# Kernel optimization log

Hardware: AMD Instinct MI355X
Metric: run time of the kernel (lower is better)

Reference implementation:

```python
import jax, jax.numpy as jnp
import numpy as np

V, E, D_ENC, H, A, NF, K = 96, 64, 256, 256, 128, 10, 5
B, T_ENC, T_TGT = 64, 1024, 256


def setup_inputs() -> dict:
    key = jax.random.key(0)
    ks = jax.random.split(key, 16)
    s = 0.05
    emb = jax.random.normal(ks[0], (V, E), jnp.float32) * s
    emb = emb.at[0].set(0.0)  # padding_idx=0
    inp = {
        "encoder_outputs": jax.random.normal(ks[1], (B, T_ENC, D_ENC), jnp.float32),
        "encoder_lengths": jax.random.randint(ks[2], (B,), 1, T_ENC + 1),
        "targets": jax.random.randint(ks[3], (B, T_TGT), 0, V),
        "emb": emb,
        "W_ih": jax.random.normal(ks[4], (4 * H, E + D_ENC), jnp.float32) * s,
        "W_hh": jax.random.normal(ks[5], (4 * H, H), jnp.float32) * s,
        "b_ih": jax.random.normal(ks[6], (4 * H,), jnp.float32) * s,
        "b_hh": jax.random.normal(ks[7], (4 * H,), jnp.float32) * s,
        "conv_w": jax.random.normal(ks[8], (NF, 1, K), jnp.float32) * s,
        "W_enc": jax.random.normal(ks[9], (A, D_ENC), jnp.float32) * s,
        "W_dec": jax.random.normal(ks[10], (A, H), jnp.float32) * s,
        "W_loc": jax.random.normal(ks[11], (A, NF), jnp.float32) * s,
        "v_w": jax.random.normal(ks[12], (1, A), jnp.float32) * s,
        "out_w1": jax.random.normal(ks[13], (H, H + D_ENC), jnp.float32) * s,
        "out_b1": jax.random.normal(ks[14], (H,), jnp.float32) * s,
        "out_w2": jax.random.normal(ks[15], (V, H), jnp.float32) * s,
        "out_b2": jnp.zeros((V,), jnp.float32),
    }
    return inp


def _forward(encoder_outputs, encoder_lengths, targets, emb, W_ih, W_hh, b_ih,
             b_hh, conv_w, W_enc, W_dec, W_loc, v_w, out_w1, out_b1, out_w2, out_b2):
    dtype = encoder_outputs.dtype
    b, t_enc, d_enc = encoder_outputs.shape
    mask = jnp.arange(t_enc)[None, :] < encoder_lengths[:, None]  # [B, T_enc]
    enc_proj = encoder_outputs @ W_enc.T  # [B, T_enc, A] (weights fixed -> hoisted)
    bias = b_ih + b_hh
    pad = (K - 1) // 2

    tok_emb = emb[targets[:, :-1]]          # [B, T_dec, E]
    tok_emb = jnp.swapaxes(tok_emb, 0, 1)   # [T_dec, B, E] for scan

    h0 = jnp.zeros((b, H), dtype)
    c0 = jnp.zeros((b, H), dtype)
    ctx0 = jnp.zeros((b, d_enc), dtype)
    aw0 = jnp.full((b, t_enc), 1.0 / t_enc, dtype)

    def step(carry, e_t):
        h, c, ctx, aw = carry
        # LSTM cell (PyTorch gate order i, f, g, o)
        x = jnp.concatenate([e_t, ctx], axis=-1)            # [B, E+D_enc]
        gates = x @ W_ih.T + h @ W_hh.T + bias              # [B, 4H]
        i, f, g, o = jnp.split(gates, 4, axis=-1)
        c = jax.nn.sigmoid(f) * c + jax.nn.sigmoid(i) * jnp.tanh(g)
        h = jax.nn.sigmoid(o) * jnp.tanh(c)
        # location-sensitive attention
        loc = jax.lax.conv_general_dilated(aw[:, None, :], conv_w, (1,),
                                           [(pad, pad)],
                                           dimension_numbers=("NCH", "OIH", "NCH"))
        loc = jnp.swapaxes(loc, 1, 2)                       # [B, T_enc, NF]
        energy_in = enc_proj + (h @ W_dec.T)[:, None, :] + loc @ W_loc.T
        energy = jnp.tanh(energy_in) @ v_w[0]               # [B, T_enc]
        energy = jnp.where(mask, energy, -1e9)
        aw = jax.nn.softmax(energy, axis=1)
        ctx = jnp.einsum("bt,btd->bd", aw, encoder_outputs)
        # output MLP (dropout = identity at eval)
        hid = jnp.tanh(jnp.concatenate([h, ctx], axis=-1) @ out_w1.T + out_b1)
        logits = hid @ out_w2.T + out_b2                    # [B, V]
        return (h, c, ctx, aw), logits

    _, logits = jax.lax.scan(step, (h0, c0, ctx0, aw0), tok_emb)
    return jnp.swapaxes(logits, 0, 1)  # [B, T_dec, V]


def reference(encoder_outputs, encoder_lengths, targets, emb, W_ih, W_hh, b_ih,
              b_hh, conv_w, W_enc, W_dec, W_loc, v_w, out_w1, out_b1, out_w2, out_b2):
    return _forward(encoder_outputs, encoder_lengths, targets, emb, W_ih, W_hh,
                    b_ih, b_hh, conv_w, W_enc, W_dec, W_loc, v_w, out_w1,
                    out_b1, out_w2, out_b2)
```

## Files before the change

### kernel.cpp

```cpp
#include <hip/hip_runtime.h>
#include <hip/hip_bf16.h>

#define BB   64
#define TENC 1024
#define DENC 256
#define HN   256
#define AN   128
#define NFC  10
#define EMBD 64
#define VN   96
#define TT   255
#define KX   576

__device__ __forceinline__ float fsig(float x){ return 1.0f/(1.0f+__expf(-x)); }
__device__ __forceinline__ float ftanh(float x){ return 1.0f - 2.0f/(1.0f+__expf(2.0f*x)); }

__global__ void k_prep(const float* __restrict__ W_ih, const float* __restrict__ W_hh,
                       const float* __restrict__ b_ih, const float* __restrict__ b_hh,
                       const float* __restrict__ W_dec,
                       float* __restrict__ Wcomb, float* __restrict__ bias,
                       float* __restrict__ WdecT, float* __restrict__ e_init,
                       float* __restrict__ S_init)
{
    int tid = blockIdx.x*blockDim.x + threadIdx.x;
    int total = blockDim.x*gridDim.x;
    for (int i = tid; i < 1024*KX; i += total){
        int g = i / KX, k = i - g*KX;
        Wcomb[i] = (k < 320) ? W_ih[g*320 + k] : W_hh[g*256 + (k-320)];
    }
    for (int i = tid; i < 1024; i += total) bias[i] = b_ih[i] + b_hh[i];
    for (int i = tid; i < 256*128; i += total){ int u = i>>7, a = i&127; WdecT[i] = W_dec[a*256 + u]; }
    for (int i = tid; i < BB*TENC; i += total) e_init[i] = 1.0f;
    for (int i = tid; i < BB; i += total) S_init[i] = (float)TENC;
}

__global__ __launch_bounds__(128) void k_encproj(const float* __restrict__ enc,
                                                 const float* __restrict__ W_enc,
                                                 float* __restrict__ enc_proj)
{
    __shared__ float rows[32][256];
    int r0 = blockIdx.x * 32;
    for (int i = threadIdx.x; i < 32*256; i += 128)
        rows[i>>8][i&255] = enc[(size_t)r0*256 + i];
    __syncthreads();
    int a = threadIdx.x;
    float acc[32];
    #pragma unroll
    for (int r=0;r<32;r++) acc[r]=0.f;
    const float* w = W_enc + a*256;
    for (int d=0; d<256; d+=4){
        float4 wv = *(const float4*)(w + d);
        #pragma unroll
        for (int r=0;r<32;r++){
            float4 rv = *(const float4*)(&rows[r][d]);
            acc[r] += wv.x*rv.x + wv.y*rv.y + wv.z*rv.z + wv.w*rv.w;
        }
    }
    for (int r=0;r<32;r++) enc_proj[(size_t)(r0+r)*AN + a] = acc[r];
}

__global__ __launch_bounds__(256) void k_att(
    const float* __restrict__ enc, const float* __restrict__ enc_proj,
    const float* __restrict__ conv_w, const float* __restrict__ W_loc,
    const float* __restrict__ v_w, const int* __restrict__ lengths,
    const float* __restrict__ WdecT, const float* __restrict__ h_cur,
    const float* __restrict__ e_prev, float* __restrict__ e_new,
    const float* __restrict__ SU_r, float* __restrict__ ctxU_w, float* __restrict__ SU_w)
{
    int b  = blockIdx.y;
    int ch = blockIdx.x;
    int t0 = ch*64;
    int tid = threadIdx.x;

    int len = lengths[b];
    int nv = len - t0; nv = nv < 0 ? 0 : (nv > 64 ? 64 : nv);
    if (nv == 0){
        if (tid < 64) e_new[b*TENC + t0 + tid] = 0.f;
        return;
    }

    __shared__ float hdec_s[128];
    __shared__ float part_s[256];
    __shared__ float ehalo[68];
    __shared__ float loc_s[64][11];
    __shared__ float cw_s[52];
    __shared__ float evals[64];
    __shared__ float ep[64][33];
    __shared__ float wacc[4][256];

    if (tid < 50) cw_s[tid] = conv_w[tid];
    for (int i = tid; i < 68; i += 256){
        int g = t0 - 2 + i;
        ehalo[i] = (g >= 0 && g < TENC) ? e_prev[b*TENC + g] : 0.f;
    }
    {
        int a = tid & 127, half = tid >> 7;
        const float* wd = WdecT + (size_t)(half*128)*AN + a;
        const float* hb = h_cur + b*HN + half*128;
        float s0 = 0.f, s1 = 0.f;
        for (int u = 0; u < 128; u += 2){
            s0 += hb[u]   * wd[(size_t)u*AN];
            s1 += hb[u+1] * wd[(size_t)(u+1)*AN];
        }
        part_s[tid] = s0 + s1;
    }
    __syncthreads();
    if (tid < 128) hdec_s[tid] = part_s[tid] + part_s[tid+128];
    float invS = 1.0f / SU_r[b];
    if (tid < 64){
        int p = tid;
        #pragma unroll
        for (int f = 0; f < NFC; f++){
            float s = 0.f;
            #pragma unroll
            for (int k = 0; k < 5; k++) s += ehalo[p+k] * cw_s[f*5+k];
            loc_s[p][f] = s * invS;
        }
    }
    __syncthreads();

    {
        int ag = tid & 31, pg = tid >> 5;
        int a0 = ag*4;
        float4 hd = *(const float4*)&hdec_s[a0];
        float4 vv = *(const float4*)(v_w + a0);
        float4 wl[NFC];
        #pragma unroll
        for (int f = 0; f < NFC; f++){
            wl[f].x = W_loc[(a0+0)*NFC + f];
            wl[f].y = W_loc[(a0+1)*NFC + f];
            wl[f].z = W_loc[(a0+2)*NFC + f];
            wl[f].w = W_loc[(a0+3)*NFC + f];
        }
        for (int i = 0; i < 8; i++){
            int p = pg*8 + i;
            if (p < nv){
                float4 er = *(const float4*)(enc_proj + (size_t)(b*TENC + t0 + p)*AN + a0);
                float x0 = er.x + hd.x, x1 = er.y + hd.y, x2 = er.z + hd.z, x3 = er.w + hd.w;
                #pragma unroll
                for (int f = 0; f < NFC; f++){
                    float lf = loc_s[p][f];
                    x0 += lf * wl[f].x; x1 += lf * wl[f].y;
                    x2 += lf * wl[f].z; x3 += lf * wl[f].w;
                }
                ep[p][ag] = vv.x*ftanh(x0) + vv.y*ftanh(x1) + vv.z*ftanh(x2) + vv.w*ftanh(x3);
            }
        }
    }
    __syncthreads();

    if (tid < 64){
        int p = tid;
        float e = 0.f;
        if (p < nv){
            float s0 = 0.f, s1 = 0.f;
            #pragma unroll
            for (int j = 0; j < 32; j += 2){ s0 += ep[p][j]; s1 += ep[p][j+1]; }
            e = __expf(s0 + s1);
        }
        evals[p] = e;
        e_new[b*TENC + t0 + p] = e;
        float se = e;
        #pragma unroll
        for (int off = 32; off; off >>= 1) se += __shfl_xor(se, off);
        if (tid == 0) atomicAdd(SU_w + b, se);
    }
    __syncthreads();

    {
        int dq = tid & 63, pq = tid >> 6;
        float4 acc = {0.f,0.f,0.f,0.f};
        for (int i = 0; i < 16; i++){
            int p = pq + i*4;
            if (p < nv){
                float ev = evals[p];
                float4 ex = *(const float4*)(enc + (size_t)(b*TENC + t0 + p)*DENC + dq*4);
                acc.x += ev*ex.x; acc.y += ev*ex.y; acc.z += ev*ex.z; acc.w += ev*ex.w;
            }
        }
        *(float4*)&wacc[pq][dq*4] = acc;
    }
    __syncthreads();
    {
        int d = tid;
        float s = wacc[0][d] + wacc[1][d] + wacc[2][d] + wacc[3][d];
        atomicAdd(ctxU_w + b*DENC + d, s);
    }
}

__global__ __launch_bounds__(256) void k_cell(
    const float* __restrict__ ctxU_r, const float* __restrict__ SU_r,
    float* __restrict__ ctxU_w, float* __restrict__ SU_w,
    const int* __restrict__ targets, const float* __restrict__ emb,
    const float* __restrict__ Wcomb, const float* __restrict__ bias,
    const float* __restrict__ h_old, float* __restrict__ h_new, float* __restrict__ c_st,
    const float* __restrict__ out_w1, const float* __restrict__ out_b1,
    const float* __restrict__ hid_prev, float* __restrict__ hid_new,
    const float* __restrict__ out_w2, const float* __restrict__ out_b2,
    float* __restrict__ out, int t)
{
    int blk = blockIdx.x, tid = threadIdx.x;
    bool do_reduce = (t >= 1 && t <= 255);
    bool do_gates  = (t <= 254);
    bool do_hid    = (t >= 1 && t <= 255);
    bool do_logits = (t >= 2);

    __shared__ float smem[16*580];
    __shared__ float invS_s[32];
    __shared__ float gates_s[16][17];

    if (blk < 256){
        int bg = blk >> 6, ug = blk & 63;
        int b0 = bg*16;
        if (ug == 1 && t <= 254){
            for (int i = tid; i < 16*DENC; i += 256) ctxU_w[b0*DENC + i] = 0.f;
            if (tid < 16) SU_w[b0 + tid] = 0.f;
        }
        if (!do_gates) return;
        float (*xh)[580] = (float(*)[580])smem;
        if (tid < 16) invS_s[tid] = do_reduce ? 1.0f/SU_r[b0+tid] : 0.f;
        for (int i = tid; i < 16*EMBD; i += 256){
            int bl = i>>6, j = i&63;
            int tok = targets[(b0+bl)*256 + t];
            xh[bl][j] = emb[tok*EMBD + j];
        }
        for (int i = tid; i < 16*HN; i += 256){
            int bl = i>>8, d = i&255;
            xh[bl][320+d] = (t == 0) ? 0.f : h_old[(b0+bl)*HN + d];
        }
        __syncthreads();
        for (int i = tid; i < 16*DENC; i += 256){
            int bl = i>>8, d = i&255;
            xh[bl][64+d] = do_reduce ? ctxU_r[(b0+bl)*DENC + d] * invS_s[bl] : 0.f;
        }
        __syncthreads();
        {
            int bl = tid & 15, row = tid >> 4;
            int gidx = row >> 2, ul = row & 3;
            int g = gidx*256 + ug*4 + ul;
            const float* wr = Wcomb + (size_t)g*KX;
            float a0 = bias[g], a1 = 0.f, a2 = 0.f, a3 = 0.f;
            for (int k = 0; k < KX; k += 4){
                float4 wv = *(const float4*)(wr + k);
                float4 xv = *(const float4*)(&xh[bl][k]);
                a0 += wv.x*xv.x; a1 += wv.y*xv.y; a2 += wv.z*xv.z; a3 += wv.w*xv.w;
            }
            gates_s[bl][row] = (a0+a1)+(a2+a3);
        }
        __syncthreads();
        if (tid < 64){
            int bl = tid >> 2, ul = tid & 3;
            int bgl = b0 + bl, ugl = ug*4 + ul;
            float gi = gates_s[bl][0*4+ul], gf = gates_s[bl][1*4+ul];
            float gg = gates_s[bl][2*4+ul], go = gates_s[bl][3*4+ul];
            float cold = (t == 0) ? 0.f : c_st[bgl*HN + ugl];
            float cn = fsig(gf)*cold + fsig(gi)*ftanh(gg);
            c_st[bgl*HN + ugl] = cn;
            h_new[bgl*HN + ugl] = fsig(go)*ftanh(cn);
        }
        return;
    }

    if (blk < 320){
        if (!do_hid) return;
        int hb = blk - 256;
        int bg = hb >> 4, rg = hb & 15;
        int b0 = bg*16;
        float (*xh2)[516] = (float(*)[516])smem;
        if (tid < 16) invS_s[tid] = 1.0f/SU_r[b0+tid];
        for (int i = tid; i < 16*HN; i += 256){
            int bl = i>>8, d = i&255;
            xh2[bl][d] = h_old[(b0+bl)*HN + d];
        }
        __syncthreads();
        for (int i = tid; i < 16*DENC; i += 256){
            int bl = i>>8, d = i&255;
            xh2[bl][256+d] = ctxU_r[(b0+bl)*DENC + d] * invS_s[bl];
        }
        __syncthreads();
        {
            int bl = tid & 15, rl = tid >> 4;
            int r = rg*16 + rl;
            const float* w1 = out_w1 + (size_t)r*512;
            float a0 = 0.f, a1 = 0.f, a2 = 0.f, a3 = 0.f;
            for (int k = 0; k < 512; k += 4){
                float4 wv = *(const float4*)(w1 + k);
                float4 xv = *(const float4*)(&xh2[bl][k]);
                a0 += wv.x*xv.x; a1 += wv.y*xv.y; a2 += wv.z*xv.z; a3 += wv.w*xv.w;
            }
            hid_new[(b0+bl)*HN + r] = ftanh(((a0+a1)+(a2+a3)) + out_b1[r]);
        }
        return;
    }

    {
        if (!do_logits) return;
        int lb = blk - 320;
        int vg = lb % 12, bgr = lb / 12;
        int b0 = bgr*32;
        float (*hs)[260] = (float(*)[260])smem;
        for (int i = tid; i < 32*HN; i += 256){
            int bl = i>>8, d = i&255;
            hs[bl][d] = hid_prev[(b0+bl)*HN + d];
        }
        __syncthreads();
        {
            int bl = tid & 31, vr = tid >> 5;
            int v = vg*8 + vr;
            const float* w2 = out_w2 + (size_t)v*HN;
            float a0 = 0.f, a1 = 0.f, a2 = 0.f, a3 = 0.f;
            for (int k = 0; k < HN; k += 4){
                float4 wv = *(const float4*)(w2 + k);
                float4 xv = *(const float4*)(&hs[bl][k]);
                a0 += wv.x*xv.x; a1 += wv.y*xv.y; a2 += wv.z*xv.z; a3 += wv.w*xv.w;
            }
            out[((size_t)(b0+bl)*TT + (t-2))*VN + v] = ((a0+a1)+(a2+a3)) + out_b2[v];
        }
    }
}

extern "C" void kernel_launch(void* const* d_in, const int* in_sizes, int n_in,
                              void* d_out, int out_size, void* d_ws, size_t ws_size,
                              hipStream_t stream)
{
    const float* enc     = (const float*)d_in[0];
    const int*   lengths = (const int*)  d_in[1];
    const int*   targets = (const int*)  d_in[2];
    const float* emb     = (const float*)d_in[3];
    const float* W_ih    = (const float*)d_in[4];
    const float* W_hh    = (const float*)d_in[5];
    const float* b_ih    = (const float*)d_in[6];
    const float* b_hh    = (const float*)d_in[7];
    const float* conv_w  = (const float*)d_in[8];
    const float* W_enc   = (const float*)d_in[9];
    const float* W_dec   = (const float*)d_in[10];
    const float* W_loc   = (const float*)d_in[11];
    const float* v_w     = (const float*)d_in[12];
    const float* out_w1  = (const float*)d_in[13];
    const float* out_b1  = (const float*)d_in[14];
    const float* out_w2  = (const float*)d_in[15];
    const float* out_b2  = (const float*)d_in[16];
    float* out = (float*)d_out;

    float* ws = (float*)d_ws;
    size_t off = 0;
    auto alloc = [&](size_t n){ float* p = ws + off; off += n; return p; };
    float* enc_proj = alloc((size_t)BB*TENC*AN);
    float* Wcomb    = alloc(1024*KX);
    float* biasw    = alloc(1024);
    float* WdecT    = alloc(256*128);
    float* e0       = alloc(BB*TENC);
    float* e1       = alloc(BB*TENC);
    float* ebuf[2]  = {e0, e1};
    float* ctxU0    = alloc(BB*DENC);
    float* ctxU1    = alloc(BB*DENC);
    float* ctxU[2]  = {ctxU0, ctxU1};
    float* SU0      = alloc(BB);
    float* SU1      = alloc(BB);
    float* SU[2]    = {SU0, SU1};
    float* h0       = alloc(BB*HN);
    float* h1       = alloc(BB*HN);
    float* hbuf[2]  = {h0, h1};
    float* c_st     = alloc(BB*HN);
    float* hidA     = alloc(BB*HN);
    float* hidB     = alloc(BB*HN);
    float* hidbuf[2] = {hidA, hidB};
    if (off * sizeof(float) > ws_size) return;

    k_prep<<<dim3(512), dim3(256), 0, stream>>>(W_ih, W_hh, b_ih, b_hh, W_dec,
                                                Wcomb, biasw, WdecT, e1, SU1);
    k_encproj<<<dim3(2048), dim3(128), 0, stream>>>(enc, W_enc, enc_proj);

    for (int t = 0; t <= 256; t++){
        k_cell<<<dim3(344), dim3(256), 0, stream>>>(
            ctxU[(t+1)&1], SU[(t+1)&1], ctxU[t&1], SU[t&1],
            targets, emb, Wcomb, biasw,
            hbuf[(t+1)&1], hbuf[t&1], c_st,
            out_w1, out_b1, hidbuf[(t+1)&1], hidbuf[t&1],
            out_w2, out_b2, out, t);
        if (t <= 254){
            k_att<<<dim3(16,64), dim3(256), 0, stream>>>(
                enc, enc_proj, conv_w, W_loc, v_w, lengths, WdecT,
                hbuf[t&1], ebuf[(t+1)&1], ebuf[t&1],
                SU[(t+1)&1], ctxU[t&1], SU[t&1]);
        }
    }
}
```

Before: 11.72 ms.

## Fuse decoder time loop into one persistent cooperative kernel with grid syncs

Replaces about 512 per-step kernel launches with one persistent cooperative kernel of 256 blocks. Each step runs a cell phase and an attention phase separated by grid-wide barriers. Weights are pre-transposed so the gate, output-MLP and logits matvecs read coalesced columns and split the K dimension across warps. Each block now handles four attention chunks, which cuts parallelism to 256 blocks in exchange for removing launch overhead. If the cooperative launch fails, the code falls back to per-step launches.

```diff
diff --git a/kernel.cpp b/kernel.cpp
--- a/kernel.cpp
+++ b/kernel.cpp
@@ -1,5 +1,8 @@
 #include <hip/hip_runtime.h>
 #include <hip/hip_bf16.h>
+#include <hip/hip_cooperative_groups.h>
+
+namespace cg = cooperative_groups;
 
 #define BB   64
 #define TENC 1024
@@ -10,28 +13,44 @@
 #define EMBD 64
 #define VN   96
 #define TT   255
-#define KX   576
 
 __device__ __forceinline__ float fsig(float x){ return 1.0f/(1.0f+__expf(-x)); }
 __device__ __forceinline__ float ftanh(float x){ return 1.0f - 2.0f/(1.0f+__expf(2.0f*x)); }
 
+struct Params {
+    const float* enc; const float* enc_proj;
+    const float* conv_w; const float* W_loc; const float* v_w;
+    const int* lengths; const int* targets; const float* emb;
+    const float* WdecT; const float* WcombP; const float* biasw;
+    const float* W1T; const float* out_b1; const float* W2T; const float* out_b2;
+    float* e0; float* e1; float* ctxU0; float* ctxU1; float* SU0; float* SU1;
+    float* h0; float* h1; float* c_st; float* hidA; float* hidB;
+    float* out;
+};
+
 __global__ void k_prep(const float* __restrict__ W_ih, const float* __restrict__ W_hh,
                        const float* __restrict__ b_ih, const float* __restrict__ b_hh,
-                       const float* __restrict__ W_dec,
-                       float* __restrict__ Wcomb, float* __restrict__ bias,
-                       float* __restrict__ WdecT, float* __restrict__ e_init,
+                       const float* __restrict__ W_dec, const float* __restrict__ out_w1,
+                       const float* __restrict__ out_w2,
+                       float* __restrict__ WcombP, float* __restrict__ biasw,
+                       float* __restrict__ WdecT, float* __restrict__ W1T,
+                       float* __restrict__ W2T, float* __restrict__ e_init,
                        float* __restrict__ S_init)
 {
     int tid = blockIdx.x*blockDim.x + threadIdx.x;
-    int total = blockDim.x*gridDim.x;
-    for (int i = tid; i < 1024*KX; i += total){
-        int g = i / KX, k = i - g*KX;
-        Wcomb[i] = (k < 320) ? W_ih[g*320 + k] : W_hh[g*256 + (k-320)];
-    }
-    for (int i = tid; i < 1024; i += total) bias[i] = b_ih[i] + b_hh[i];
-    for (int i = tid; i < 256*128; i += total){ int u = i>>7, a = i&127; WdecT[i] = W_dec[a*256 + u]; }
-    for (int i = tid; i < BB*TENC; i += total) e_init[i] = 1.0f;
-    for (int i = tid; i < BB; i += total) S_init[i] = (float)TENC;
+    int tot = blockDim.x*gridDim.x;
+    for (int i = tid; i < 576*1024; i += tot){
+        int k = i >> 10, rp = i & 1023;
+        int ug = rp >> 4, q = rp & 15, gidx = q >> 2, ul = q & 3;
+        int g = gidx*256 + ug*4 + ul;
+        WcombP[i] = (k < 320) ? W_ih[(size_t)g*320 + k] : W_hh[(size_t)g*256 + (k-320)];
+    }
+    for (int i = tid; i < 1024; i += tot) biasw[i] = b_ih[i] + b_hh[i];
+    for (int i = tid; i < 256*128; i += tot){ int u = i>>7, a = i&127; WdecT[i] = W_dec[a*256 + u]; }
+    for (int i = tid; i < 512*256; i += tot){ int k = i>>8, r = i&255; W1T[i] = out_w1[(size_t)r*512 + k]; }
+    for (int i = tid; i < 256*96;  i += tot){ int k = i/96, v = i - k*96; W2T[i] = out_w2[(size_t)v*256 + k]; }
+    for (int i = tid; i < BB*TENC; i += tot) e_init[i] = 1.0f;
+    for (int i = tid; i < BB; i += tot) S_init[i] = (float)TENC;
 }
 
 __global__ __launch_bounds__(128) void k_encproj(const float* __restrict__ enc,
@@ -59,264 +78,306 @@
     for (int r=0;r<32;r++) enc_proj[(size_t)(r0+r)*AN + a] = acc[r];
 }
 
-__global__ __launch_bounds__(256) void k_att(
-    const float* __restrict__ enc, const float* __restrict__ enc_proj,
-    const float* __restrict__ conv_w, const float* __restrict__ W_loc,
-    const float* __restrict__ v_w, const int* __restrict__ lengths,
-    const float* __restrict__ WdecT, const float* __restrict__ h_cur,
-    const float* __restrict__ e_prev, float* __restrict__ e_new,
-    const float* __restrict__ SU_r, float* __restrict__ ctxU_w, float* __restrict__ SU_w)
-{
-    int b  = blockIdx.y;
-    int ch = blockIdx.x;
-    int t0 = ch*64;
-    int tid = threadIdx.x;
-
-    int len = lengths[b];
-    int nv = len - t0; nv = nv < 0 ? 0 : (nv > 64 ? 64 : nv);
-    if (nv == 0){
-        if (tid < 64) e_new[b*TENC + t0 + tid] = 0.f;
-        return;
-    }
-
-    __shared__ float hdec_s[128];
-    __shared__ float part_s[256];
-    __shared__ float ehalo[68];
-    __shared__ float loc_s[64][11];
-    __shared__ float cw_s[52];
-    __shared__ float evals[64];
-    __shared__ float ep[64][33];
-    __shared__ float wacc[4][256];
-
-    if (tid < 50) cw_s[tid] = conv_w[tid];
-    for (int i = tid; i < 68; i += 256){
-        int g = t0 - 2 + i;
-        ehalo[i] = (g >= 0 && g < TENC) ? e_prev[b*TENC + g] : 0.f;
-    }
+union alignas(16) SMem {
+    struct { float hdec[128]; float part[256]; float ehalo[68]; float loc[64][11];
+             float cw[52]; float evals[64]; float ep[64][33]; float wacc[4][256]; } att;
+    struct { float xh[8][584]; float part[4][16][9]; float gates[8][17]; } gat;
+    struct { float xh[8][520]; float part[4][16][9]; } hidm;
+    struct { float hs[8][260]; float part[4][32][9]; } lgt;
+};
+
+__device__ __forceinline__ void cell_phase(const Params& P, int t, int blk, int tid, SMem& u)
+{
+    const int wr = t & 1;
+    const float* ctxU_r = wr ? P.ctxU0 : P.ctxU1;
+    float*       ctxU_w = wr ? P.ctxU1 : P.ctxU0;
+    const float* SU_r   = wr ? P.SU0   : P.SU1;
+    float*       SU_w   = wr ? P.SU1   : P.SU0;
+    const float* h_old  = wr ? P.h0    : P.h1;
+    float*       h_new  = wr ? P.h1    : P.h0;
+    const float* hid_pv = wr ? P.hidA  : P.hidB;
+    float*       hid_nw = wr ? P.hidB  : P.hidA;
+
+    for (int half = 0; half < 2; half++){
+        if (t > 254) break;
+        const int vb = blk + (half << 8);
+        const int ug = vb & 63, bg = vb >> 6;
+        const int b0 = bg*8;
+        if (ug == 1){
+            for (int i = tid; i < 8*DENC; i += 256) ctxU_w[b0*DENC + i] = 0.f;
+            if (tid < 8) SU_w[b0 + tid] = 0.f;
+        }
+        for (int i = tid; i < 8*EMBD; i += 256){
+            int bl = i>>6, j = i&63;
+            int tok = P.targets[(b0+bl)*256 + t];
+            u.gat.xh[bl][j] = P.emb[tok*EMBD + j];
+        }
+        for (int i = tid; i < 8*HN; i += 256){
+            int bl = i>>8, d = i&255;
+            u.gat.xh[bl][320+d] = (t == 0) ? 0.f : h_old[(b0+bl)*HN + d];
+        }
+        for (int i = tid; i < 8*DENC; i += 256){
+            int bl = i>>8, d = i&255;
+            u.gat.xh[bl][64+d] = (t == 0) ? 0.f
+                : ctxU_r[(b0+bl)*DENC + d] * (1.0f/SU_r[b0+bl]);
+        }
+        __syncthreads();
+        {
+            const int kq = tid >> 6, lane = tid & 63, rl = lane & 15, blq = lane >> 4;
+            const int rowP = ug*16 + rl, bl0 = blq*2;
+            const float* wp  = P.WcombP + (size_t)(kq*144)*1024 + rowP;
+            const float* x0p = &u.gat.xh[bl0][kq*144];
+            const float* x1p = &u.gat.xh[bl0+1][kq*144];
+            float s0 = 0.f, s1 = 0.f;
+            for (int k = 0; k < 144; k += 4){
+                float w0 = wp[0], w1 = wp[1024], w2 = wp[2048], w3 = wp[3072]; wp += 4096;
+                float4 xa = *(const float4*)(x0p + k);
+                float4 xb = *(const float4*)(x1p + k);
+                s0 += w0*xa.x + w1*xa.y + w2*xa.z + w3*xa.w;
+                s1 += w0*xb.x + w1*xb.y + w2*xb.z + w3*xb.w;
+            }
+            u.gat.part[kq][rl][bl0] = s0; u.gat.part[kq][rl][bl0+1] = s1;
+        }
+        __syncthreads();
+        if (tid < 128){
+            int bl = tid >> 4, rl = tid & 15;
+            float s = u.gat.part[0][rl][bl] + u.gat.part[1][rl][bl]
+                    + u.gat.part[2][rl][bl] + u.gat.part[3][rl][bl];
+            int gidx = rl >> 2, ul = rl & 3;
+            u.gat.gates[bl][rl] = s + P.biasw[gidx*256 + ug*4 + ul];
+        }
+        __syncthreads();
+        if (tid < 32){
+            int bl = tid >> 2, ul = tid & 3;
+            int bgl = b0 + bl, unit = ug*4 + ul;
+            float gi = u.gat.gates[bl][0+ul],  gf = u.gat.gates[bl][4+ul];
+            float gg = u.gat.gates[bl][8+ul],  go = u.gat.gates[bl][12+ul];
+            float cold = (t == 0) ? 0.f : P.c_st[bgl*HN + unit];
+            float cn = fsig(gf)*cold + fsig(gi)*ftanh(gg);
+            P.c_st[bgl*HN + unit] = cn;
+            h_new[bgl*HN + unit] = fsig(go)*ftanh(cn);
+        }
+        __syncthreads();
+    }
+
+    if (blk < 128 && t >= 1 && t <= 255){
+        int bg = blk >> 4, rg = blk & 15;
+        int b0 = bg*8, r0 = rg*16;
+        for (int i = tid; i < 8*HN; i += 256){
+            int bl = i>>8, d = i&255;
+            u.hidm.xh[bl][d] = h_old[(b0+bl)*HN + d];
+        }
+        for (int i = tid; i < 8*DENC; i += 256){
+            int bl = i>>8, d = i&255;
+            u.hidm.xh[bl][256+d] = ctxU_r[(b0+bl)*DENC + d] * (1.0f/SU_r[b0+bl]);
+        }
+        __syncthreads();
+        {
+            const int kq = tid >> 6, lane = tid & 63, rl = lane & 15, blq = lane >> 4;
+            const int bl0 = blq*2;
+            const float* wp  = P.W1T + (size_t)(kq*128)*256 + (r0 + rl);
+            const float* x0p = &u.hidm.xh[bl0][kq*128];
+            const float* x1p = &u.hidm.xh[bl0+1][kq*128];
+            float s0 = 0.f, s1 = 0.f;
+            for (int k = 0; k < 128; k += 4){
+                float w0 = wp[0], w1 = wp[256], w2 = wp[512], w3 = wp[768]; wp += 1024;
+                float4 xa = *(const float4*)(x0p + k);
+                float4 xb = *(const float4*)(x1p + k);
+                s0 += w0*xa.x + w1*xa.y + w2*xa.z + w3*xa.w;
+                s1 += w0*xb.x + w1*xb.y + w2*xb.z + w3*xb.w;
+            }
+            u.hidm.part[kq][rl][bl0] = s0; u.hidm.part[kq][rl][bl0+1] = s1;
+        }
+        __syncthreads();
+        if (tid < 128){
+            int bl = tid >> 4, rl = tid & 15;
+            int r = r0 + rl;
+            float s = u.hidm.part[0][rl][bl] + u.hidm.part[1][rl][bl]
+                    + u.hidm.part[2][rl][bl] + u.hidm.part[3][rl][bl];
+            hid_nw[(b0+bl)*HN + r] = ftanh(s + P.out_b1[r]);
+        }
+        __syncthreads();
+    }
+
+    if (blk >= 128 && blk < 152 && t >= 2){
+        int lt = blk - 128;
+        int bgr = lt/3, vg = lt%3;
+        int b0 = bgr*8, v0 = vg*32;
+        for (int i = tid; i < 8*HN; i += 256){
+            int bl = i>>8, d = i&255;
+            u.lgt.hs[bl][d] = hid_pv[(b0+bl)*HN + d];
+        }
+        __syncthreads();
+        {
+            const int kq = tid >> 6, lane = tid & 63, vl = lane & 31, blq = lane >> 5;
+            const int bl0 = blq*4;
+            const float* wp = P.W2T + (size_t)(kq*64)*96 + (v0 + vl);
+            float a4[4] = {0.f,0.f,0.f,0.f};
+            for (int k = 0; k < 64; k += 4){
+                float w0 = wp[0], w1 = wp[96], w2 = wp[192], w3 = wp[288]; wp += 384;
+                #pragma unroll
+                for (int j = 0; j < 4; j++){
+                    float4 x = *(const float4*)&u.lgt.hs[bl0+j][kq*64 + k];
+                    a4[j] += w0*x.x + w1*x.y + w2*x.z + w3*x.w;
+                }
+            }
+            #pragma unroll
+            for (int j = 0; j < 4; j++) u.lgt.part[kq][vl][bl0+j] = a4[j];
+        }
+        __syncthreads();
+        {
+            int bl = tid >> 5, vl = tid & 31;
+            int v = v0 + vl;
+            float s = u.lgt.part[0][vl][bl] + u.lgt.part[1][vl][bl]
+                    + u.lgt.part[2][vl][bl] + u.lgt.part[3][vl][bl];
+            P.out[((size_t)(b0+bl)*TT + (t-2))*VN + v] = s + P.out_b2[v];
+        }
+        __syncthreads();
+    }
+}
+
+__device__ __forceinline__ void att_phase(const Params& P, int t, int blk, int tid, SMem& u)
+{
+    if (t > 254) return;
+    const int wr = t & 1;
+    float*       ctxU_w = wr ? P.ctxU1 : P.ctxU0;
+    const float* SU_r   = wr ? P.SU0   : P.SU1;
+    float*       SU_w   = wr ? P.SU1   : P.SU0;
+    const float* h_new  = wr ? P.h1    : P.h0;
+    const float* e_prev = wr ? P.e0    : P.e1;
+    float*       e_new  = wr ? P.e1    : P.e0;
+
+    const int b_att = blk & 63, cq = blk >> 6;
+    const int ag = tid & 31, pg = tid >> 5;
+    const int a0 = ag*4;
+    float4 vv = *(const float4*)(P.v_w + a0);
+    float4 wl[NFC];
+    #pragma unroll
+    for (int f = 0; f < NFC; f++){
+        wl[f].x = P.W_loc[(a0+0)*NFC+f]; wl[f].y = P.W_loc[(a0+1)*NFC+f];
+        wl[f].z = P.W_loc[(a0+2)*NFC+f]; wl[f].w = P.W_loc[(a0+3)*NFC+f];
+    }
+    const int len_att = P.lengths[b_att];
+
+    if (tid < 50) u.att.cw[tid] = P.conv_w[tid];
     {
         int a = tid & 127, half = tid >> 7;
-        const float* wd = WdecT + (size_t)(half*128)*AN + a;
-        const float* hb = h_cur + b*HN + half*128;
+        const float* wd  = P.WdecT + (size_t)(half*128)*AN + a;
+        const float* hbp = h_new + b_att*HN + half*128;
         float s0 = 0.f, s1 = 0.f;
-        for (int u = 0; u < 128; u += 2){
-            s0 += hb[u]   * wd[(size_t)u*AN];
-            s1 += hb[u+1] * wd[(size_t)(u+1)*AN];
-        }
-        part_s[tid] = s0 + s1;
+        for (int uu = 0; uu < 128; uu += 2){
+            s0 += hbp[uu]   * wd[(size_t)uu*AN];
+            s1 += hbp[uu+1] * wd[(size_t)(uu+1)*AN];
+        }
+        u.att.part[tid] = s0 + s1;
     }
     __syncthreads();
-    if (tid < 128) hdec_s[tid] = part_s[tid] + part_s[tid+128];
-    float invS = 1.0f / SU_r[b];
-    if (tid < 64){
-        int p = tid;
-        #pragma unroll
-        for (int f = 0; f < NFC; f++){
-            float s = 0.f;
+    if (tid < 128) u.att.hdec[tid] = u.att.part[tid] + u.att.part[tid+128];
+    __syncthreads();
+    float4 hd4 = *(const float4*)&u.att.hdec[a0];
+    float invS = 1.0f / SU_r[b_att];
+
+    for (int kk = 0; kk < 4; kk++){
+        int ch = cq + 4*kk;
+        int t0 = ch*64;
+        int nv = len_att - t0; nv = nv < 0 ? 0 : (nv > 64 ? 64 : nv);
+        if (nv == 0){
+            if (tid < 64) e_new[b_att*TENC + t0 + tid] = 0.f;
+            continue;
+        }
+        __syncthreads();
+        if (tid < 68){
+            int g = t0 - 2 + tid;
+            u.att.ehalo[tid] = (g >= 0 && g < TENC) ? e_prev[b_att*TENC + g] : 0.f;
+        }
+        __syncthreads();
+        if (tid < 64){
             #pragma unroll
-            for (int k = 0; k < 5; k++) s += ehalo[p+k] * cw_s[f*5+k];
-            loc_s[p][f] = s * invS;
-        }
-    }
-    __syncthreads();
-
-    {
-        int ag = tid & 31, pg = tid >> 5;
-        int a0 = ag*4;
-        float4 hd = *(const float4*)&hdec_s[a0];
-        float4 vv = *(const float4*)(v_w + a0);
-        float4 wl[NFC];
-        #pragma unroll
-        for (int f = 0; f < NFC; f++){
-            wl[f].x = W_loc[(a0+0)*NFC + f];
-            wl[f].y = W_loc[(a0+1)*NFC + f];
-            wl[f].z = W_loc[(a0+2)*NFC + f];
-            wl[f].w = W_loc[(a0+3)*NFC + f];
-        }
+            for (int f = 0; f < NFC; f++){
+                float s = 0.f;
+                #pragma unroll
+                for (int k2 = 0; k2 < 5; k2++) s += u.att.ehalo[tid+k2] * u.att.cw[f*5+k2];
+                u.att.loc[tid][f] = s * invS;
+            }
+        }
+        __syncthreads();
+        const float* epr = P.enc_proj + (size_t)(b_att*TENC + t0)*AN;
         for (int i = 0; i < 8; i++){
             int p = pg*8 + i;
             if (p < nv){
-                float4 er = *(const float4*)(enc_proj + (size_t)(b*TENC + t0 + p)*AN + a0);
-                float x0 = er.x + hd.x, x1 = er.y + hd.y, x2 = er.z + hd.z, x3 = er.w + hd.w;
+                float4 er = *(const float4*)(epr + (size_t)p*AN + a0);
+                float x0 = er.x + hd4.x, x1 = er.y + hd4.y;
+                float x2 = er.z + hd4.z, x3 = er.w + hd4.w;
                 #pragma unroll
                 for (int f = 0; f < NFC; f++){
-                    float lf = loc_s[p][f];
-                    x0 += lf * wl[f].x; x1 += lf * wl[f].y;
-                    x2 += lf * wl[f].z; x3 += lf * wl[f].w;
+                    float lf = u.att.loc[p][f];
+                    x0 += lf*wl[f].x; x1 += lf*wl[f].y;
+                    x2 += lf*wl[f].z; x3 += lf*wl[f].w;
                 }
-                ep[p][ag] = vv.x*ftanh(x0) + vv.y*ftanh(x1) + vv.z*ftanh(x2) + vv.w*ftanh(x3);
-            }
-        }
-    }
-    __syncthreads();
-
-    if (tid < 64){
-        int p = tid;
-        float e = 0.f;
-        if (p < nv){
-            float s0 = 0.f, s1 = 0.f;
+                u.att.ep[p][ag] = vv.x*ftanh(x0) + vv.y*ftanh(x1)
+                                + vv.z*ftanh(x2) + vv.w*ftanh(x3);
+            }
+        }
+        __syncthreads();
+        if (tid < 64){
+            float e = 0.f;
+            if (tid < nv){
+                float s0 = 0.f, s1 = 0.f;
+                #pragma unroll
+                for (int j = 0; j < 32; j += 2){ s0 += u.att.ep[tid][j]; s1 += u.att.ep[tid][j+1]; }
+                e = __expf(s0 + s1);
+            }
+            u.att.evals[tid] = e;
+            e_new[b_att*TENC + t0 + tid] = e;
+            float se = e;
             #pragma unroll
-            for (int j = 0; j < 32; j += 2){ s0 += ep[p][j]; s1 += ep[p][j+1]; }
-            e = __expf(s0 + s1);
-        }
-        evals[p] = e;
-        e_new[b*TENC + t0 + p] = e;
-        float se = e;
-        #pragma unroll
-        for (int off = 32; off; off >>= 1) se += __shfl_xor(se, off);
-        if (tid == 0) atomicAdd(SU_w + b, se);
-    }
-    __syncthreads();
-
-    {
-        int dq = tid & 63, pq = tid >> 6;
-        float4 acc = {0.f,0.f,0.f,0.f};
-        for (int i = 0; i < 16; i++){
-            int p = pq + i*4;
-            if (p < nv){
-                float ev = evals[p];
-                float4 ex = *(const float4*)(enc + (size_t)(b*TENC + t0 + p)*DENC + dq*4);
-                acc.x += ev*ex.x; acc.y += ev*ex.y; acc.z += ev*ex.z; acc.w += ev*ex.w;
-            }
-        }
-        *(float4*)&wacc[pq][dq*4] = acc;
-    }
-    __syncthreads();
-    {
-        int d = tid;
-        float s = wacc[0][d] + wacc[1][d] + wacc[2][d] + wacc[3][d];
-        atomicAdd(ctxU_w + b*DENC + d, s);
-    }
-}
-
-__global__ __launch_bounds__(256) void k_cell(
-    const float* __restrict__ ctxU_r, const float* __restrict__ SU_r,
-    float* __restrict__ ctxU_w, float* __restrict__ SU_w,
-    const int* __restrict__ targets, const float* __restrict__ emb,
-    const float* __restrict__ Wcomb, const float* __restrict__ bias,
-    const float* __restrict__ h_old, float* __restrict__ h_new, float* __restrict__ c_st,
-    const float* __restrict__ out_w1, const float* __restrict__ out_b1,
-    const float* __restrict__ hid_prev, float* __restrict__ hid_new,
-    const float* __restrict__ out_w2, const float* __restrict__ out_b2,
-    float* __restrict__ out, int t)
-{
-    int blk = blockIdx.x, tid = threadIdx.x;
-    bool do_reduce = (t >= 1 && t <= 255);
-    bool do_gates  = (t <= 254);
-    bool do_hid    = (t >= 1 && t <= 255);
-    bool do_logits = (t >= 2);
-
-    __shared__ float smem[16*580];
-    __shared__ float invS_s[32];
-    __shared__ float gates_s[16][17];
-
-    if (blk < 256){
-        int bg = blk >> 6, ug = blk & 63;
-        int b0 = bg*16;
-        if (ug == 1 && t <= 254){
-            for (int i = tid; i < 16*DENC; i += 256) ctxU_w[b0*DENC + i] = 0.f;
-            if (tid < 16) SU_w[b0 + tid] = 0.f;
-        }
-        if (!do_gates) return;
-        float (*xh)[580] = (float(*)[580])smem;
-        if (tid < 16) invS_s[tid] = do_reduce ? 1.0f/SU_r[b0+tid] : 0.f;
-        for (int i = tid; i < 16*EMBD; i += 256){
-            int bl = i>>6, j = i&63;
-            int tok = targets[(b0+bl)*256 + t];
-            xh[bl][j] = emb[tok*EMBD + j];
-        }
-        for (int i = tid; i < 16*HN; i += 256){
-            int bl = i>>8, d = i&255;
-            xh[bl][320+d] = (t == 0) ? 0.f : h_old[(b0+bl)*HN + d];
-        }
-        __syncthreads();
-        for (int i = tid; i < 16*DENC; i += 256){
-            int bl = i>>8, d = i&255;
-            xh[bl][64+d] = do_reduce ? ctxU_r[(b0+bl)*DENC + d] * invS_s[bl] : 0.f;
+            for (int off = 32; off; off >>= 1) se += __shfl_xor(se, off);
+            if (tid == 0) atomicAdd(SU_w + b_att, se);
         }
         __syncthreads();
         {
-            int bl = tid & 15, row = tid >> 4;
-            int gidx = row >> 2, ul = row & 3;
-            int g = gidx*256 + ug*4 + ul;
-            const float* wr = Wcomb + (size_t)g*KX;
-            float a0 = bias[g], a1 = 0.f, a2 = 0.f, a3 = 0.f;
-            for (int k = 0; k < KX; k += 4){
-                float4 wv = *(const float4*)(wr + k);
-                float4 xv = *(const float4*)(&xh[bl][k]);
-                a0 += wv.x*xv.x; a1 += wv.y*xv.y; a2 += wv.z*xv.z; a3 += wv.w*xv.w;
-            }
-            gates_s[bl][row] = (a0+a1)+(a2+a3);
-        }
-        __syncthreads();
-        if (tid < 64){
-            int bl = tid >> 2, ul = tid & 3;
-            int bgl = b0 + bl, ugl = ug*4 + ul;
-            float gi = gates_s[bl][0*4+ul], gf = gates_s[bl][1*4+ul];
-            float gg = gates_s[bl][2*4+ul], go = gates_s[bl][3*4+ul];
-            float cold = (t == 0) ? 0.f : c_st[bgl*HN + ugl];
-            float cn = fsig(gf)*cold + fsig(gi)*ftanh(gg);
-            c_st[bgl*HN + ugl] = cn;
-            h_new[bgl*HN + ugl] = fsig(go)*ftanh(cn);
-        }
-        return;
-    }
-
-    if (blk < 320){
-        if (!do_hid) return;
-        int hb = blk - 256;
-        int bg = hb >> 4, rg = hb & 15;
-        int b0 = bg*16;
-        float (*xh2)[516] = (float(*)[516])smem;
-        if (tid < 16) invS_s[tid] = 1.0f/SU_r[b0+tid];
-        for (int i = tid; i < 16*HN; i += 256){
-            int bl = i>>8, d = i&255;
-            xh2[bl][d] = h_old[(b0+bl)*HN + d];
-        }
-        __syncthreads();
-        for (int i = tid; i < 16*DENC; i += 256){
-            int bl = i>>8, d = i&255;
-            xh2[bl][256+d] = ctxU_r[(b0+bl)*DENC + d] * invS_s[bl];
-        }
-        __syncthreads();
-        {
-            int bl = tid & 15, rl = tid >> 4;
-            int r = rg*16 + rl;
-            const float* w1 = out_w1 + (size_t)r*512;
-            float a0 = 0.f, a1 = 0.f, a2 = 0.f, a3 = 0.f;
-            for (int k = 0; k < 512; k += 4){
-                float4 wv = *(const float4*)(w1 + k);
-                float4 xv = *(const float4*)(&xh2[bl][k]);
-                a0 += wv.x*xv.x; a1 += wv.y*xv.y; a2 += wv.z*xv.z; a3 += wv.w*xv.w;
-            }
-            hid_new[(b0+bl)*HN + r] = ftanh(((a0+a1)+(a2+a3)) + out_b1[r]);
-        }
-        return;
-    }
-
-    {
-        if (!do_logits) return;
-        int lb = blk - 320;
-        int vg = lb % 12, bgr = lb / 12;
-        int b0 = bgr*32;
-        float (*hs)[260] = (float(*)[260])smem;
-        for (int i = tid; i < 32*HN; i += 256){
-            int bl = i>>8, d = i&255;
-            hs[bl][d] = hid_prev[(b0+bl)*HN + d];
-        }
-        __syncthreads();
-        {
-            int bl = tid & 31, vr = tid >> 5;
-            int v = vg*8 + vr;
-            const float* w2 = out_w2 + (size_t)v*HN;
-            float a0 = 0.f, a1 = 0.f, a2 = 0.f, a3 = 0.f;
-            for (int k = 0; k < HN; k += 4){
-                float4 wv = *(const float4*)(w2 + k);
-                float4 xv = *(const float4*)(&hs[bl][k]);
-                a0 += wv.x*xv.x; a1 += wv.y*xv.y; a2 += wv.z*xv.z; a3 += wv.w*xv.w;
-            }
-            out[((size_t)(b0+bl)*TT + (t-2))*VN + v] = ((a0+a1)+(a2+a3)) + out_b2[v];
-        }
-    }
+            int dq = tid & 63, pq = tid >> 6;
+            float4 acc = {0.f,0.f,0.f,0.f};
+            const float* encb = P.enc + (size_t)(b_att*TENC + t0)*DENC;
+            for (int i = 0; i < 16; i++){
+                int p = pq + i*4;
+                if (p < nv){
+                    float ev = u.att.evals[p];
+                    float4 ex = *(const float4*)(encb + (size_t)p*DENC + dq*4);
+                    acc.x += ev*ex.x; acc.y += ev*ex.y;
+                    acc.z += ev*ex.z; acc.w += ev*ex.w;
+                }
+            }
+            *(float4*)&u.att.wacc[pq][dq*4] = acc;
+        }
+        __syncthreads();
+        atomicAdd(ctxU_w + b_att*DENC + tid,
+                  u.att.wacc[0][tid] + u.att.wacc[1][tid]
+                + u.att.wacc[2][tid] + u.att.wacc[3][tid]);
+    }
+}
+
+__global__ __launch_bounds__(256, 1) void k_loop(Params P)
+{
+    cg::grid_group grid = cg::this_grid();
+    __shared__ SMem u;
+    for (int t = 0; t <= 256; t++){
+        cell_phase(P, t, blockIdx.x, threadIdx.x, u);
+        grid.sync();
+        att_phase(P, t, blockIdx.x, threadIdx.x, u);
+        grid.sync();
+    }
+}
+
+__global__ __launch_bounds__(256, 1) void k_cell_step(Params P, int t)
+{
+    __shared__ SMem u;
+    cell_phase(P, t, blockIdx.x, threadIdx.x, u);
+}
+__global__ __launch_bounds__(256, 1) void k_att_step(Params P, int t)
+{
+    __shared__ SMem u;
+    att_phase(P, t, blockIdx.x, threadIdx.x, u);
 }
 
 extern "C" void kernel_launch(void* const* d_in, const int* in_sizes, int n_in,
@@ -346,43 +407,46 @@
     size_t off = 0;
     auto alloc = [&](size_t n){ float* p = ws + off; off += n; return p; };
     float* enc_proj = alloc((size_t)BB*TENC*AN);
-    float* Wcomb    = alloc(1024*KX);
+    float* WcombP   = alloc(576*1024);
     float* biasw    = alloc(1024);
     float* WdecT    = alloc(256*128);
+    float* W1T      = alloc(512*256);
+    float* W2T      = alloc(256*96);
     float* e0       = alloc(BB*TENC);
     float* e1       = alloc(BB*TENC);
-    float* ebuf[2]  = {e0, e1};
     float* ctxU0    = alloc(BB*DENC);
     float* ctxU1    = alloc(BB*DENC);
-    float* ctxU[2]  = {ctxU0, ctxU1};
     float* SU0      = alloc(BB);
     float* SU1      = alloc(BB);
-    float* SU[2]    = {SU0, SU1};
     float* h0       = alloc(BB*HN);
     float* h1       = alloc(BB*HN);
-    float* hbuf[2]  = {h0, h1};
     float* c_st     = alloc(BB*HN);
     float* hidA     = alloc(BB*HN);
     float* hidB     = alloc(BB*HN);
-    float* hidbuf[2] = {hidA, hidB};
     if (off * sizeof(float) > ws_size) return;
 
-    k_prep<<<dim3(512), dim3(256), 0, stream>>>(W_ih, W_hh, b_ih, b_hh, W_dec,
-                                                Wcomb, biasw, WdecT, e1, SU1);
+    k_prep<<<dim3(512), dim3(256), 0, stream>>>(W_ih, W_hh, b_ih, b_hh, W_dec, out_w1, out_w2,
+                                                WcombP, biasw, WdecT, W1T, W2T, e1, SU1);
     k_encproj<<<dim3(2048), dim3(128), 0, stream>>>(enc, W_enc, enc_proj);
 
-    for (int t = 0; t <= 256; t++){
-        k_cell<<<dim3(344), dim3(256), 0, stream>>>(
-            ctxU[(t+1)&1], SU[(t+1)&1], ctxU[t&1], SU[t&1],
-            targets, emb, Wcomb, biasw,
-            hbuf[(t+1)&1], hbuf[t&1], c_st,
-            out_w1, out_b1, hidbuf[(t+1)&1], hidbuf[t&1],
-            out_w2, out_b2, out, t);
-        if (t <= 254){
-            k_att<<<dim3(16,64), dim3(256), 0, stream>>>(
-                enc, enc_proj, conv_w, W_loc, v_w, lengths, WdecT,
-                hbuf[t&1], ebuf[(t+1)&1], ebuf[t&1],
-                SU[(t+1)&1], ctxU[t&1], SU[t&1]);
-        }
-    }
-}
+    Params pr;
+    pr.enc = enc; pr.enc_proj = enc_proj;
+    pr.conv_w = conv_w; pr.W_loc = W_loc; pr.v_w = v_w;
+    pr.lengths = lengths; pr.targets = targets; pr.emb = emb;
+    pr.WdecT = WdecT; pr.WcombP = WcombP; pr.biasw = biasw;
+    pr.W1T = W1T; pr.out_b1 = out_b1; pr.W2T = W2T; pr.out_b2 = out_b2;
+    pr.e0 = e0; pr.e1 = e1; pr.ctxU0 = ctxU0; pr.ctxU1 = ctxU1;
+    pr.SU0 = SU0; pr.SU1 = SU1; pr.h0 = h0; pr.h1 = h1;
+    pr.c_st = c_st; pr.hidA = hidA; pr.hidB = hidB; pr.out = out;
+
+    void* args[] = { (void*)&pr };
+    hipError_t err = hipLaunchCooperativeKernel((const void*)k_loop, dim3(256), dim3(256),
+                                                args, 0, stream);
+    if (err != hipSuccess){
+        for (int t = 0; t <= 256; t++){
+            k_cell_step<<<dim3(256), dim3(256), 0, stream>>>(pr, t);
+            if (t <= 254)
+                k_att_step<<<dim3(256), dim3(256), 0, stream>>>(pr, t);
+        }
+    }
+}
```

After: 39.43 ms. 236% more time.
